# Kernel optimization log

Hardware: AMD Instinct MI355X
Metric: run time of the kernel (lower is better)

Reference implementation:

```python
import jax, jax.numpy as jnp
import numpy as np

TAU_S = 3.0
DT_MAX = 5.0
BATCH, N, D = 64, 16384, 256


def setup_inputs() -> dict:
    key = jax.random.key(0)
    k1, k2, k3 = jax.random.split(key, 3)
    # query spike times in [0, 20) ms, matching the pattern_times range (5, 20)
    query_times = jax.random.uniform(k1, (BATCH, D), dtype=jnp.float32) * 20.0
    patterns = jax.random.normal(k2, (N, D), dtype=jnp.float32) * 0.1
    weights = jnp.ones((D,), dtype=jnp.float32)
    return {"query_times": query_times, "patterns": patterns, "weights": weights}


def reference(query_times, patterns, weights):
    # pattern spike times in (5, 20) ms
    pattern_times = 20.0 - 15.0 * jax.nn.sigmoid(patterns)  # (N, d)
    # broadcast difference: (batch, N, d)
    dt = query_times[:, None, :] - pattern_times[None, :, :]
    adt = jnp.abs(dt)
    # temporal kernel: exp decay inside coincidence window, zero outside
    kappa = jnp.where(adt < DT_MAX, jnp.exp(-adt / TAU_S), 0.0)
    w = jnp.abs(weights)  # (d,)
    # weighted reduce over d -> (batch, N)
    S = jnp.einsum("bnd,d->bn", kappa, w)
    return S
```

## Files before the change

kernel.cpp:

```cpp
#include <hip/hip_runtime.h>
#include <hip/hip_bf16.h>


#include <stdint.h>

typedef _Float16 h2  __attribute__((ext_vector_type(2)));
typedef short    s2v __attribute__((ext_vector_type(2)));

static constexpr float kC2    = 0.48089834696298783f;
static constexpr float kL2E   = 1.4426950408889634f;
static constexpr float kTheta = 0.18887560283756183f;

#define B_   64
#define N_   16384
#define D_   256
#define NCH  64
#define NTL  256

union HU { uint32_t u; h2 h; s2v s; };
__device__ __forceinline__ h2 uh(uint32_t x) { HU c; c.u = x; return c.h; }

__global__ __launch_bounds__(256) void pre_pattern(const float* __restrict__ patterns,
                                                   uint4* __restrict__ pat2) {
    const int nt = blockIdx.x >> 2;
    const int qq = blockIdx.x & 3;
#pragma unroll
    for (int it = 0; it < 4; ++it) {
        int g   = qq * 1024 + it * 256 + threadIdx.x;
        int dc  = g >> 6;
        int row = g & 63;
        float4 x4 = *(const float4*)&patterns[((size_t)nt * 64 + row) * D_ + dc * 4];
        float xs[4] = {x4.x, x4.y, x4.z, x4.w};
        union { uint4 u; _Float16 h[8]; } o;
#pragma unroll
        for (int j = 0; j < 4; ++j) {
            float t  = exp2f(-xs[j] * kL2E);
            float sg = __fdividef(1.0f, 1.0f + t);
            float u  = fmaf(-15.0f * kC2, sg, 20.0f * kC2);
            o.h[j]     = (_Float16)exp2f(u);
            o.h[4 + j] = (_Float16)exp2f(-u);
        }
        pat2[(size_t)nt * 4096 + dc * 64 + row] = o.u;
    }
}

__global__ __launch_bounds__(256) void pre_query(const float* __restrict__ q,
                                                 const float* __restrict__ w,
                                                 _Float16* __restrict__ qh,
                                                 _Float16* __restrict__ wh) {
    const int b = blockIdx.x;
    const int d = threadIdx.x;
    float qv = q[(size_t)b * D_ + d];
    float u  = qv * kC2;
    int dc = d >> 2, p = (d >> 1) & 1, hh = d & 1, bg2 = b >> 1, b2 = b & 1;
    size_t base = (size_t)(dc * 32 + bg2) * 16;
    qh[base + (size_t)(b2 * 2 + p) * 2 + hh]     = (_Float16)exp2f(u);
    qh[base + 8 + (size_t)(b2 * 2 + p) * 2 + hh] = (_Float16)exp2f(-u);
    if (b == 0) {
        float wa = fabsf(w[d]);
        wh[dc * 8 + p * 2 + hh]     = (_Float16)(kTheta * wa);
        wh[dc * 8 + 4 + p * 2 + hh] = (_Float16)wa;
    }
}

struct QB { uint32_t eq[4]; uint32_t iq[4]; };
struct WB { uint32_t tw[2]; uint32_t w[2]; };

__device__ __forceinline__ void load_q(const uint32_t* __restrict__ qarr,
                                       const uint32_t* __restrict__ wtab,
                                       int dc, int bg2, QB& o, WB& wo) {
    const uint32_t* p = qarr + (size_t)(dc * 32 + bg2) * 8;
#pragma unroll
    for (int j = 0; j < 4; ++j) o.eq[j] = p[j];
#pragma unroll
    for (int j = 0; j < 4; ++j) o.iq[j] = p[4 + j];
    const uint32_t* wp = wtab + dc * 4;
    wo.tw[0] = wp[0]; wo.tw[1] = wp[1]; wo.w[0] = wp[2]; wo.w[1] = wp[3];
}

__device__ __forceinline__ void chunk_math(const QB& Q, const WB& W, uint4 P,
                                           float acc[2]) {
    h2 ep[2] = {uh(P.x), uh(P.y)};
    h2 ip[2] = {uh(P.z), uh(P.w)};
#pragma unroll
    for (int b2 = 0; b2 < 2; ++b2) {
#pragma unroll
        for (int p = 0; p < 2; ++p) {
            h2 a = uh(Q.eq[b2 * 2 + p]) * ip[p];
            h2 c = uh(Q.iq[b2 * 2 + p]) * ep[p];
            h2 m = __builtin_elementwise_min(a, c);
            h2 t = uh(W.tw[p]) - m;
            HU tm; tm.h = t;
            tm.s = tm.s >> 15;
            HU mm; mm.h = m;
            mm.u &= tm.u;
#if __has_builtin(__builtin_amdgcn_fdot2)
            acc[b2] = __builtin_amdgcn_fdot2(mm.h, uh(W.w[p]), acc[b2], false);
#else
            h2 wp2 = uh(W.w[p]);
            acc[b2] = fmaf((float)mm.h.x, (float)wp2.x,
                      fmaf((float)mm.h.y, (float)wp2.y, acc[b2]));
#endif
        }
    }
}

__global__ __launch_bounds__(256, 8) void cd_main(
        const uint4* __restrict__ pat2,
        const uint32_t* __restrict__ qarr,
        const uint32_t* __restrict__ wtab,
        float* __restrict__ S) {
    const int l    = threadIdx.x & 63;
    const int wv   = threadIdx.x >> 6;
    const int nt   = blockIdx.x & 255;
    const int bsub = blockIdx.x >> 8;
    const int bg2  = __builtin_amdgcn_readfirstlane(bsub * 4 + wv);
    const int b0   = bg2 * 2;

    const uint4* pbase = pat2 + (size_t)nt * 4096 + l;

    float acc[2] = {0.f, 0.f};

    QB qA, qB; WB wA, wB;
    uint4 pA, pB;
    load_q(qarr, wtab, 0, bg2, qA, wA);
    pA = pbase[0];

    for (int dc = 0; dc < NCH - 2; dc += 2) {
        load_q(qarr, wtab, dc + 1, bg2, qB, wB);
        pB = pbase[(dc + 1) * 64];
        chunk_math(qA, wA, pA, acc);
        load_q(qarr, wtab, dc + 2, bg2, qA, wA);
        pA = pbase[(dc + 2) * 64];
        chunk_math(qB, wB, pB, acc);
    }
    load_q(qarr, wtab, NCH - 1, bg2, qB, wB);
    pB = pbase[(NCH - 1) * 64];
    chunk_math(qA, wA, pA, acc);
    chunk_math(qB, wB, pB, acc);

    S[(size_t)b0 * N_ + nt * 64 + l]       = acc[0];
    S[(size_t)(b0 + 1) * N_ + nt * 64 + l] = acc[1];
}

extern "C" void kernel_launch(void* const* d_in, const int* in_sizes, int n_in,
                              void* d_out, int out_size, void* d_ws, size_t ws_size,
                              hipStream_t stream) {
    const float* q        = (const float*)d_in[0];
    const float* patterns = (const float*)d_in[1];
    const float* weights  = (const float*)d_in[2];
    float* S = (float*)d_out;

    uint32_t* qarr = (uint32_t*)d_ws;
    uint32_t* wtab = (uint32_t*)((char*)d_ws + 65536);
    uint4*    pat2 = (uint4*)((char*)d_ws + 65536 + 1024);

    pre_pattern<<<NTL * 4, 256, 0, stream>>>(patterns, pat2);
    pre_query  <<<B_,      256, 0, stream>>>(q, weights,
                                             (_Float16*)qarr, (_Float16*)wtab);
    cd_main    <<<2048,    256, 0, stream>>>(pat2, qarr, wtab, S);
}
```

Measured before the change: 110.7 us.

## Fuse pattern preprocessing into main kernel via swizzled LDS tile, 4 batches per wave

Removes the separate pre_pattern kernel. Each block now converts its 64 pattern rows into half-precision exp pairs and stores them in a 64 KB XOR-swizzled shared-memory tile, then reads them from LDS instead of a global workspace. Blocks grow to 512 threads and each wave handles 4 batches instead of 2, which cuts redundant pattern transcendentals and the global round trip. In exchange it adds a barrier and higher register and LDS pressure, which lowers occupancy.

```diff
diff --git a/kernel.cpp b/kernel.cpp
--- a/kernel.cpp
+++ b/kernel.cpp
@@ -1,8 +1,6 @@
 #include <hip/hip_runtime.h>
-#include <hip/hip_bf16.h>
+#include <stdint.h>
 
-
-#include <stdint.h>
 
 typedef _Float16 h2  __attribute__((ext_vector_type(2)));
 typedef short    s2v __attribute__((ext_vector_type(2)));
@@ -15,20 +13,87 @@
 #define N_   16384
 #define D_   256
 #define NCH  64
-#define NTL  256
 
 union HU { uint32_t u; h2 h; s2v s; };
 __device__ __forceinline__ h2 uh(uint32_t x) { HU c; c.u = x; return c.h; }
 
-__global__ __launch_bounds__(256) void pre_pattern(const float* __restrict__ patterns,
-                                                   uint4* __restrict__ pat2) {
-    const int nt = blockIdx.x >> 2;
-    const int qq = blockIdx.x & 3;
+__global__ __launch_bounds__(256) void pre_query(const float* __restrict__ q,
+                                                 const float* __restrict__ w,
+                                                 _Float16* __restrict__ qh,
+                                                 _Float16* __restrict__ wh) {
+    const int b = blockIdx.x;
+    const int d = threadIdx.x;
+    float qv = q[(size_t)b * D_ + d];
+    float u  = qv * kC2;
+    int dc = d >> 2, p = (d >> 1) & 1, hh = d & 1, bg = b >> 2, b4 = b & 3;
+    size_t base = (size_t)(dc * 16 + bg) * 32;
+    qh[base + (size_t)(b4 * 2 + p) * 2 + hh]      = (_Float16)exp2f(u);
+    qh[base + 16 + (size_t)(b4 * 2 + p) * 2 + hh] = (_Float16)exp2f(-u);
+    if (b == 0) {
+        float wa = fabsf(w[d]);
+        wh[dc * 8 + p * 2 + hh]     = (_Float16)(kTheta * wa);
+        wh[dc * 8 + 4 + p * 2 + hh] = (_Float16)wa;
+    }
+}
+
+struct QB { uint32_t eq[8]; uint32_t iq[8]; };
+struct WB { uint32_t tw[2]; uint32_t w[2]; };
+
+__device__ __forceinline__ void load_q(const uint32_t* __restrict__ qarr,
+                                       const uint32_t* __restrict__ wtab,
+                                       int dc, int bg, QB& o, WB& wo) {
+    const uint32_t* p = qarr + (size_t)(dc * 16 + bg) * 16;
 #pragma unroll
-    for (int it = 0; it < 4; ++it) {
-        int g   = qq * 1024 + it * 256 + threadIdx.x;
-        int dc  = g >> 6;
-        int row = g & 63;
+    for (int j = 0; j < 8; ++j) o.eq[j] = p[j];
+#pragma unroll
+    for (int j = 0; j < 8; ++j) o.iq[j] = p[8 + j];
+    const uint32_t* wp = wtab + dc * 4;
+    wo.tw[0] = wp[0]; wo.tw[1] = wp[1]; wo.w[0] = wp[2]; wo.w[1] = wp[3];
+}
+
+__device__ __forceinline__ void chunk_math(const QB& Q, const WB& W, uint4 P,
+                                           float acc[4]) {
+    h2 ep[2] = {uh(P.x), uh(P.y)};
+    h2 ip[2] = {uh(P.z), uh(P.w)};
+#pragma unroll
+    for (int b4 = 0; b4 < 4; ++b4) {
+#pragma unroll
+        for (int p = 0; p < 2; ++p) {
+            h2 a = uh(Q.eq[b4 * 2 + p]) * ip[p];
+            h2 c = uh(Q.iq[b4 * 2 + p]) * ep[p];
+            h2 m = __builtin_elementwise_min(a, c);
+            h2 t = uh(W.tw[p]) - m;
+            HU tm; tm.h = t;
+            tm.s = tm.s >> 15;
+            HU mm; mm.h = m;
+            mm.u &= tm.u;
+#if __has_builtin(__builtin_amdgcn_fdot2)
+            acc[b4] = __builtin_amdgcn_fdot2(mm.h, uh(W.w[p]), acc[b4], false);
+#else
+            h2 wp2 = uh(W.w[p]);
+            acc[b4] = fmaf((float)mm.h.x, (float)wp2.x,
+                      fmaf((float)mm.h.y, (float)wp2.y, acc[b4]));
+#endif
+        }
+    }
+}
+
+__global__ __launch_bounds__(512, 4) void cd_main(
+        const float* __restrict__ patterns,
+        const uint32_t* __restrict__ qarr,
+        const uint32_t* __restrict__ wtab,
+        float* __restrict__ S) {
+    __shared__ uint4 sT[64][64];
+
+    const int tid = threadIdx.x;
+    const int nt  = blockIdx.x & 255;
+    const int bh  = blockIdx.x >> 8;
+
+#pragma unroll
+    for (int it = 0; it < 8; ++it) {
+        int g   = it * 512 + tid;
+        int row = g >> 6;
+        int dc  = g & 63;
         float4 x4 = *(const float4*)&patterns[((size_t)nt * 64 + row) * D_ + dc * 4];
         float xs[4] = {x4.x, x4.y, x4.z, x4.w};
         union { uint4 u; _Float16 h[8]; } o;
@@ -40,107 +105,39 @@
             o.h[j]     = (_Float16)exp2f(u);
             o.h[4 + j] = (_Float16)exp2f(-u);
         }
-        pat2[(size_t)nt * 4096 + dc * 64 + row] = o.u;
+        sT[row][dc ^ (row & 7)] = o.u;
     }
-}
+    __syncthreads();
 
-__global__ __launch_bounds__(256) void pre_query(const float* __restrict__ q,
-                                                 const float* __restrict__ w,
-                                                 _Float16* __restrict__ qh,
-                                                 _Float16* __restrict__ wh) {
-    const int b = blockIdx.x;
-    const int d = threadIdx.x;
-    float qv = q[(size_t)b * D_ + d];
-    float u  = qv * kC2;
-    int dc = d >> 2, p = (d >> 1) & 1, hh = d & 1, bg2 = b >> 1, b2 = b & 1;
-    size_t base = (size_t)(dc * 32 + bg2) * 16;
-    qh[base + (size_t)(b2 * 2 + p) * 2 + hh]     = (_Float16)exp2f(u);
-    qh[base + 8 + (size_t)(b2 * 2 + p) * 2 + hh] = (_Float16)exp2f(-u);
-    if (b == 0) {
-        float wa = fabsf(w[d]);
-        wh[dc * 8 + p * 2 + hh]     = (_Float16)(kTheta * wa);
-        wh[dc * 8 + 4 + p * 2 + hh] = (_Float16)wa;
-    }
-}
+    const int l  = tid & 63;
+    const int wv = tid >> 6;
+    const int bg = __builtin_amdgcn_readfirstlane(bh * 8 + wv);
+    const int b0 = bg * 4;
+    const int lx = l & 7;
 
-struct QB { uint32_t eq[4]; uint32_t iq[4]; };
-struct WB { uint32_t tw[2]; uint32_t w[2]; };
-
-__device__ __forceinline__ void load_q(const uint32_t* __restrict__ qarr,
-                                       const uint32_t* __restrict__ wtab,
-                                       int dc, int bg2, QB& o, WB& wo) {
-    const uint32_t* p = qarr + (size_t)(dc * 32 + bg2) * 8;
-#pragma unroll
-    for (int j = 0; j < 4; ++j) o.eq[j] = p[j];
-#pragma unroll
-    for (int j = 0; j < 4; ++j) o.iq[j] = p[4 + j];
-    const uint32_t* wp = wtab + dc * 4;
-    wo.tw[0] = wp[0]; wo.tw[1] = wp[1]; wo.w[0] = wp[2]; wo.w[1] = wp[3];
-}
-
-__device__ __forceinline__ void chunk_math(const QB& Q, const WB& W, uint4 P,
-                                           float acc[2]) {
-    h2 ep[2] = {uh(P.x), uh(P.y)};
-    h2 ip[2] = {uh(P.z), uh(P.w)};
-#pragma unroll
-    for (int b2 = 0; b2 < 2; ++b2) {
-#pragma unroll
-        for (int p = 0; p < 2; ++p) {
-            h2 a = uh(Q.eq[b2 * 2 + p]) * ip[p];
-            h2 c = uh(Q.iq[b2 * 2 + p]) * ep[p];
-            h2 m = __builtin_elementwise_min(a, c);
-            h2 t = uh(W.tw[p]) - m;
-            HU tm; tm.h = t;
-            tm.s = tm.s >> 15;
-            HU mm; mm.h = m;
-            mm.u &= tm.u;
-#if __has_builtin(__builtin_amdgcn_fdot2)
-            acc[b2] = __builtin_amdgcn_fdot2(mm.h, uh(W.w[p]), acc[b2], false);
-#else
-            h2 wp2 = uh(W.w[p]);
-            acc[b2] = fmaf((float)mm.h.x, (float)wp2.x,
-                      fmaf((float)mm.h.y, (float)wp2.y, acc[b2]));
-#endif
-        }
-    }
-}
-
-__global__ __launch_bounds__(256, 8) void cd_main(
-        const uint4* __restrict__ pat2,
-        const uint32_t* __restrict__ qarr,
-        const uint32_t* __restrict__ wtab,
-        float* __restrict__ S) {
-    const int l    = threadIdx.x & 63;
-    const int wv   = threadIdx.x >> 6;
-    const int nt   = blockIdx.x & 255;
-    const int bsub = blockIdx.x >> 8;
-    const int bg2  = __builtin_amdgcn_readfirstlane(bsub * 4 + wv);
-    const int b0   = bg2 * 2;
-
-    const uint4* pbase = pat2 + (size_t)nt * 4096 + l;
-
-    float acc[2] = {0.f, 0.f};
+    float acc[4] = {0.f, 0.f, 0.f, 0.f};
 
     QB qA, qB; WB wA, wB;
     uint4 pA, pB;
-    load_q(qarr, wtab, 0, bg2, qA, wA);
-    pA = pbase[0];
+    load_q(qarr, wtab, 0, bg, qA, wA);
+    pA = sT[l][0 ^ lx];
 
     for (int dc = 0; dc < NCH - 2; dc += 2) {
-        load_q(qarr, wtab, dc + 1, bg2, qB, wB);
-        pB = pbase[(dc + 1) * 64];
+        load_q(qarr, wtab, dc + 1, bg, qB, wB);
+        pB = sT[l][(dc + 1) ^ lx];
         chunk_math(qA, wA, pA, acc);
-        load_q(qarr, wtab, dc + 2, bg2, qA, wA);
-        pA = pbase[(dc + 2) * 64];
+        load_q(qarr, wtab, dc + 2, bg, qA, wA);
+        pA = sT[l][(dc + 2) ^ lx];
         chunk_math(qB, wB, pB, acc);
     }
-    load_q(qarr, wtab, NCH - 1, bg2, qB, wB);
-    pB = pbase[(NCH - 1) * 64];
+    load_q(qarr, wtab, NCH - 1, bg, qB, wB);
+    pB = sT[l][(NCH - 1) ^ lx];
     chunk_math(qA, wA, pA, acc);
     chunk_math(qB, wB, pB, acc);
 
-    S[(size_t)b0 * N_ + nt * 64 + l]       = acc[0];
-    S[(size_t)(b0 + 1) * N_ + nt * 64 + l] = acc[1];
+#pragma unroll
+    for (int i = 0; i < 4; ++i)
+        S[(size_t)(b0 + i) * N_ + nt * 64 + l] = acc[i];
 }
 
 extern "C" void kernel_launch(void* const* d_in, const int* in_sizes, int n_in,
@@ -153,10 +150,7 @@
 
     uint32_t* qarr = (uint32_t*)d_ws;
     uint32_t* wtab = (uint32_t*)((char*)d_ws + 65536);
-    uint4*    pat2 = (uint4*)((char*)d_ws + 65536 + 1024);
 
-    pre_pattern<<<NTL * 4, 256, 0, stream>>>(patterns, pat2);
-    pre_query  <<<B_,      256, 0, stream>>>(q, weights,
-                                             (_Float16*)qarr, (_Float16*)wtab);
-    cd_main    <<<2048,    256, 0, stream>>>(pat2, qarr, wtab, S);
+    pre_query<<<B_, 256, 0, stream>>>(q, weights, (_Float16*)qarr, (_Float16*)wtab);
+    cd_main  <<<512, 512, 0, stream>>>(patterns, qarr, wtab, S);
 }
```

Measured after the change: 109.5 us. Within noise of the previous version (-1.1%).
